# Optimization experiments

Measured on AMD Instinct MI355X. Metric: run time of the kernel, lower is better.

Reference implementation:

```python
import jax, jax.numpy as jnp
import numpy as np

A, B, D, H, O = 64, 4096, 50, 192, 3

def _xavier(key, shape, gain=0.5):
    fan_in, fan_out = shape[-1], shape[-2]
    limit = gain * np.sqrt(6.0 / (fan_in + fan_out))
    return jax.random.uniform(key, shape, jnp.float32, -limit, limit)

def setup_inputs() -> dict:
    key = jax.random.key(0)
    ks = jax.random.split(key, 12)
    return {
        "x": jax.random.normal(ks[0], (B, D), jnp.float32),
        "input_norm_weight": _xavier(ks[1], (A, D)),
        "input_norm_bias": jnp.zeros((A, D), jnp.float32),
        "layer1_weight": _xavier(ks[2], (A, H, D)),
        "layer1_bias": jnp.zeros((A, H), jnp.float32),
        "layer2_weight": _xavier(ks[3], (A, H, H)),
        "layer2_bias": jnp.zeros((A, H), jnp.float32),
        "layer3_weight": _xavier(ks[4], (A, H, H)),
        "layer3_bias": jnp.zeros((A, H), jnp.float32),
        "output_weight": _xavier(ks[5], (A, O, H)),
        "output_bias": jnp.zeros((A, O), jnp.float32),
        "skip1_weight": _xavier(ks[6], (A, H, D)),
        "skip1_bias": jnp.zeros((A, H), jnp.float32),
        "skip2_weight": _xavier(ks[7], (A, H, H)),
        "skip2_bias": jnp.zeros((A, H), jnp.float32),
        "hidden_norm_weight": _xavier(ks[8], (A, H)),
        "hidden_norm_bias": jnp.zeros((A, H), jnp.float32),
    }

def reference(x, input_norm_weight, input_norm_bias,
              layer1_weight, layer1_bias, layer2_weight, layer2_bias,
              layer3_weight, layer3_bias, output_weight, output_bias,
              skip1_weight, skip1_bias, skip2_weight, skip2_bias,
              hidden_norm_weight, hidden_norm_bias):
    # NOTE: the vectorized ensemble's "norms" are affine-only (no mean/var), per source.
    # x: [B, D] -> broadcast over agents: [A, B, D]
    x_norm = x[None, :, :] * input_norm_weight[:, None, :] + input_norm_bias[:, None, :]
    gelu = lambda t: jax.nn.gelu(t, approximate=False)  # torch F.gelu exact
    # per-agent GEMMs: [A,B,in] x [A,out,in] -> [A,B,out]
    h1 = gelu(jnp.einsum('abi,ahi->abh', x_norm, layer1_weight) + layer1_bias[:, None, :]) \
         + jnp.einsum('abi,ahi->abh', x_norm, skip1_weight) + skip1_bias[:, None, :]
    h2 = gelu(jnp.einsum('abi,ahi->abh', h1, layer2_weight) + layer2_bias[:, None, :]) \
         + jnp.einsum('abi,ahi->abh', h1, skip2_weight) + skip2_bias[:, None, :]
    h3 = jnp.einsum('abi,ahi->abh', h2, layer3_weight) + layer3_bias[:, None, :] + h2
    h3 = h3 * hidden_norm_weight[:, None, :] + hidden_norm_bias[:, None, :]
    logits = jnp.einsum('abh,aoh->abo', h3, output_weight) + output_bias[:, None, :]
    return logits  # [A, B, O]
```

## Files before the change

### kernel.cpp

```cpp
#include <hip/hip_runtime.h>
#include <math.h>

#define A_N 64
#define B_N 4096
#define D_N 50
#define H_N 192
#define O_N 3

typedef __attribute__((ext_vector_type(8))) __bf16 bf16x8;
typedef __attribute__((ext_vector_type(4))) __bf16 bf16x4;
typedef __attribute__((ext_vector_type(4))) float f32x4;

#define W1_OFF   0
#define S1_OFF   786432
#define W2_OFF   1572864
#define S2_OFF   3932160
#define W3_OFF   6291456
#define OW_OFF   8650752
#define WS_ELEMS 8847360

#if __has_builtin(__builtin_amdgcn_rcpf)
#define FRCP(x) __builtin_amdgcn_rcpf(x)
#else
#define FRCP(x) (1.0f / (x))
#endif
#if __has_builtin(__builtin_amdgcn_exp2f)
#define FEXP2(x) __builtin_amdgcn_exp2f(x)
#else
#define FEXP2(x) exp2f(x)
#endif

__device__ __forceinline__ float gelu_f(float xx) {
    float t  = 0.70710678118654752440f * xx;
    float at = fabsf(t);
    float k  = FRCP(fmaf(0.3275911f, at, 1.0f));
    float p  = fmaf(k, 1.061405429f, -1.453152027f);
    p = fmaf(k, p, 1.421413741f);
    p = fmaf(k, p, -0.284496736f);
    p = fmaf(k, p, 0.254829592f);
    p = p * k;
    float e  = FEXP2(t * t * -1.44269504088896340736f);
    float er = fmaf(-p, e, 1.0f);
    er = (t < 0.f) ? -er : er;
    return 0.5f * xx * (1.0f + er);
}

__global__ __launch_bounds__(256)
void prep_kernel(const float* __restrict__ w1, const float* __restrict__ s1,
                 const float* __restrict__ w2, const float* __restrict__ s2,
                 const float* __restrict__ w3, const float* __restrict__ ow,
                 __bf16* __restrict__ ws) {
    __shared__ __bf16 T[192 * 72];
    const int b   = blockIdx.x;
    const int tid = threadIdx.x;

    if (b < 1152) {
        int m  = b / 384;
        int r  = b % 384;
        int a  = r / 6;
        int rc = r % 6;
        const float* src = ((m == 0) ? w2 : (m == 1) ? s2 : w3) + (size_t)a * 36864;
        __bf16* dst = ws + ((m == 0) ? W2_OFF : (m == 1) ? S2_OFF : W3_OFF) + (size_t)a * 36864;
        #pragma unroll
        for (int i = 0; i < 6; ++i) {
            int f4 = i * 256 + tid;
            int row = f4 / 48, kc = (f4 % 48) * 4;
            f32x4 v = *(const f32x4*)(src + (size_t)(rc * 32 + row) * 192 + kc);
            bf16x4 o;
            #pragma unroll
            for (int j = 0; j < 4; ++j) o[j] = (__bf16)v[j];
            *(bf16x4*)(T + row * 200 + kc) = o;
        }
        __syncthreads();
        #pragma unroll
        for (int i = 0; i < 3; ++i) {
            int fr = i * 256 + tid;
            int f = fr >> 6, lane = fr & 63;
            int ntl = f / 6, ks = f % 6;
            int n = ntl * 16 + (lane & 15), k = ks * 32 + (lane >> 4) * 8;
            bf16x8 v = *(const bf16x8*)(T + n * 200 + k);
            *(bf16x8*)(dst + ((size_t)(rc * 2 + ntl) * 6 + ks) * 512 + lane * 8) = v;
        }
    } else if (b < 1280) {
        int r = b - 1152; int m = r >> 6; int a = r & 63;
        const float* src = (m ? s1 : w1) + (size_t)a * 9600;
        __bf16* dst = ws + (m ? S1_OFF : W1_OFF) + (size_t)a * 12288;
        for (int e = tid; e < 192 * 72; e += 256) T[e] = (__bf16)0.f;
        __syncthreads();
        for (int e = tid; e < 9600; e += 256) {
            int row = e / 50, k = e - row * 50;
            T[row * 72 + k] = (__bf16)src[e];
        }
        __syncthreads();
        #pragma unroll
        for (int i = 0; i < 6; ++i) {
            int fr = i * 256 + tid;
            int f = fr >> 6, lane = fr & 63;
            int nt = f >> 1, ks = f & 1;
            int n = nt * 16 + (lane & 15), k = ks * 32 + (lane >> 4) * 8;
            bf16x8 v = *(const bf16x8*)(T + n * 72 + k);
            *(bf16x8*)(dst + (size_t)(nt * 2 + ks) * 512 + lane * 8) = v;
        }
    } else {
        int r = b - 1280;
        #pragma unroll
        for (int i = 0; i < 8; ++i) {
            int fr = (r * 8 + i) * 256 + tid;
            int a = fr / 384, rem = fr - a * 384;
            int ks = rem >> 6, lane = rem & 63;
            int n = lane & 15, k = ks * 32 + (lane >> 4) * 8;
            bf16x8 v;
            if (n < O_N) {
                const float* p = ow + ((size_t)a * O_N + n) * H_N + k;
                f32x4 f0 = *(const f32x4*)p, f1 = *(const f32x4*)(p + 4);
                #pragma unroll
                for (int j = 0; j < 4; ++j) { v[j] = (__bf16)f0[j]; v[4 + j] = (__bf16)f1[j]; }
            } else {
                #pragma unroll
                for (int j = 0; j < 8; ++j) v[j] = (__bf16)0.f;
            }
            *(bf16x8*)(ws + OW_OFF + (size_t)a * 3072 + ks * 512 + lane * 8) = v;
        }
    }
}

#define MFMA(a, b, c) __builtin_amdgcn_mfma_f32_16x16x32_bf16((a), (b), (c), 0, 0, 0)

__global__ __launch_bounds__(256, 3)
void srek_mfma(const float* __restrict__ x,
               const float* __restrict__ inw, const float* __restrict__ inb,
               const float* __restrict__ b1,  const float* __restrict__ b2,
               const float* __restrict__ b3,  const float* __restrict__ s1b,
               const float* __restrict__ s2b, const float* __restrict__ hnw,
               const float* __restrict__ hnb, const float* __restrict__ ob,
               const __bf16* __restrict__ ws, float* __restrict__ out) {
    __shared__ __bf16 Xs[8 * 512];
    __shared__ __bf16 Hs[24 * 512];

    const int bid  = blockIdx.x;
    const int slot = bid >> 3;
    const int tile = slot & 63;
    const int a    = ((bid & 7) << 3) | (slot >> 6);
    const int row0 = tile * 64;

    const int tid  = threadIdx.x;
    const int lane = tid & 63;
    const int wv   = tid >> 6;
    const int ln   = lane & 15;
    const int quad = lane >> 4;
    const int aH   = a * H_N;
    const int c0   = wv * 48;
    const int l8   = lane * 8;
    const int f3   = wv * 3;

    const __bf16* W1 = ws + W1_OFF + (size_t)a * 12288;
    const __bf16* S1 = ws + S1_OFF + (size_t)a * 12288;
    const __bf16* W2 = ws + W2_OFF + (size_t)a * 36864;
    const __bf16* S2 = ws + S2_OFF + (size_t)a * 36864;
    const __bf16* W3 = ws + W3_OFF + (size_t)a * 36864;
    const __bf16* OWp= ws + OW_OFF + (size_t)a * 3072;

    bf16x8 nxt[6];
    f32x4 accT[12], accS[12], h2f[12];
    const f32x4 zero = {0.f, 0.f, 0.f, 0.f};

    #pragma unroll
    for (int t = 0; t < 3; ++t) {
        nxt[t]     = *(const bf16x8*)(W1 + ((f3 + t) * 2 + 0) * 512 + l8);
        nxt[3 + t] = *(const bf16x8*)(S1 + ((f3 + t) * 2 + 0) * 512 + l8);
    }

    for (int e = tid; e < 8 * 512; e += 256) {
        int j   = e & 7;
        int lnn = (e >> 3) & 15;
        int qd  = (e >> 7) & 3;
        int kss = (e >> 9) & 1;
        int mtt = (e >> 10) & 3;
        int r = mtt * 16 + lnn;
        int k = kss * 32 + qd * 8 + j;
        float v = 0.f;
        if (k < D_N) v = x[(size_t)(row0 + r) * D_N + k] * inw[a * D_N + k] + inb[a * D_N + k];
        Xs[e] = (__bf16)v;
    }

    auto compute_dual = [&](const __bf16* As, int KS, int ks,
                            const bf16x8* cw, const bf16x8* cs) {
        #pragma unroll
        for (int mt = 0; mt < 4; ++mt) {
            bf16x8 av = *(const bf16x8*)(As + (mt * KS + ks) * 512 + l8);
            #pragma unroll
            for (int t = 0; t < 3; ++t) {
                accT[mt * 3 + t] = MFMA(cw[t], av, accT[mt * 3 + t]);
                accS[mt * 3 + t] = MFMA(cs[t], av, accS[mt * 3 + t]);
            }
        }
    };
    auto compute_single = [&](int ks, const bf16x8* cw) {
        #pragma unroll
        for (int mt = 0; mt < 4; ++mt) {
            bf16x8 av = *(const bf16x8*)(Hs + (mt * 6 + ks) * 512 + l8);
            #pragma unroll
            for (int t = 0; t < 3; ++t)
                accT[mt * 3 + t] = MFMA(cw[t], av, accT[mt * 3 + t]);
        }
    };
    auto store_fragmajor = [&](const f32x4* src) {
        #pragma unroll
        for (int t = 0; t < 3; ++t) {
            int ks2 = (3 * wv + t) >> 1;
            int qp  = (6 * wv + 2 * t + (quad >> 1)) & 3;
            int off = (qp * 16 + ln) * 8 + (quad & 1) * 4;
            #pragma unroll
            for (int mt = 0; mt < 4; ++mt) {
                bf16x4 o;
                #pragma unroll
                for (int rg = 0; rg < 4; ++rg) o[rg] = (__bf16)src[mt * 3 + t][rg];
                *(bf16x4*)(Hs + (mt * 6 + ks2) * 512 + off) = o;
            }
        }
    };

    #pragma unroll
    for (int i = 0; i < 12; ++i) { accT[i] = zero; accS[i] = zero; }
    __syncthreads();

    {
        bf16x8 cw[3], cs[3];
        #pragma unroll
        for (int t = 0; t < 3; ++t) { cw[t] = nxt[t]; cs[t] = nxt[3 + t]; }
        #pragma unroll
        for (int t = 0; t < 3; ++t) {
            nxt[t]     = *(const bf16x8*)(W1 + ((f3 + t) * 2 + 1) * 512 + l8);
            nxt[3 + t] = *(const bf16x8*)(S1 + ((f3 + t) * 2 + 1) * 512 + l8);
        }
        compute_dual(Xs, 2, 0, cw, cs);
        #pragma unroll
        for (int t = 0; t < 3; ++t) { cw[t] = nxt[t]; cs[t] = nxt[3 + t]; }
        #pragma unroll
        for (int t = 0; t < 3; ++t) {
            nxt[t]     = *(const bf16x8*)(W2 + ((f3 + t) * 6 + 0) * 512 + l8);
            nxt[3 + t] = *(const bf16x8*)(S2 + ((f3 + t) * 6 + 0) * 512 + l8);
        }
        compute_dual(Xs, 2, 1, cw, cs);
    }
    #pragma unroll
    for (int t = 0; t < 3; ++t) {
        int colb = c0 + t * 16 + quad * 4;
        f32x4 bb = *(const f32x4*)(b1 + aH + colb);
        f32x4 sb = *(const f32x4*)(s1b + aH + colb);
        #pragma unroll
        for (int mt = 0; mt < 4; ++mt)
            #pragma unroll
            for (int rg = 0; rg < 4; ++rg)
                h2f[mt * 3 + t][rg] = gelu_f(accT[mt * 3 + t][rg] + bb[rg]) + accS[mt * 3 + t][rg] + sb[rg];
    }
    store_fragmajor(h2f);
    #pragma unroll
    for (int i = 0; i < 12; ++i) { accT[i] = zero; accS[i] = zero; }
    __syncthreads();

    #pragma unroll
    for (int ks = 0; ks < 6; ++ks) {
        bf16x8 cw[3], cs[3];
        #pragma unroll
        for (int t = 0; t < 3; ++t) { cw[t] = nxt[t]; cs[t] = nxt[3 + t]; }
        if (ks < 5) {
            #pragma unroll
            for (int t = 0; t < 3; ++t) {
                nxt[t]     = *(const bf16x8*)(W2 + ((f3 + t) * 6 + ks + 1) * 512 + l8);
                nxt[3 + t] = *(const bf16x8*)(S2 + ((f3 + t) * 6 + ks + 1) * 512 + l8);
            }
        } else {
            #pragma unroll
            for (int t = 0; t < 3; ++t)
                nxt[t] = *(const bf16x8*)(W3 + ((f3 + t) * 6 + 0) * 512 + l8);
        }
        compute_dual(Hs, 6, ks, cw, cs);
    }
    #pragma unroll
    for (int t = 0; t < 3; ++t) {
        int colb = c0 + t * 16 + quad * 4;
        f32x4 bb = *(const f32x4*)(b2 + aH + colb);
        f32x4 sb = *(const f32x4*)(s2b + aH + colb);
        #pragma unroll
        for (int mt = 0; mt < 4; ++mt)
            #pragma unroll
            for (int rg = 0; rg < 4; ++rg)
                h2f[mt * 3 + t][rg] = gelu_f(accT[mt * 3 + t][rg] + bb[rg]) + accS[mt * 3 + t][rg] + sb[rg];
    }
    #pragma unroll
    for (int i = 0; i < 12; ++i) accT[i] = zero;
    __syncthreads();
    store_fragmajor(h2f);
    __syncthreads();

    bf16x8 ow6[6];
    #pragma unroll
    for (int ks = 0; ks < 6; ++ks) {
        bf16x8 cw[3];
        #pragma unroll
        for (int t = 0; t < 3; ++t) cw[t] = nxt[t];
        if (ks < 5) {
            #pragma unroll
            for (int t = 0; t < 3; ++t)
                nxt[t] = *(const bf16x8*)(W3 + ((f3 + t) * 6 + ks + 1) * 512 + l8);
        } else {
            #pragma unroll
            for (int kk = 0; kk < 6; ++kk)
                ow6[kk] = *(const bf16x8*)(OWp + kk * 512 + l8);
        }
        compute_single(ks, cw);
    }
    #pragma unroll
    for (int t = 0; t < 3; ++t) {
        int colb = c0 + t * 16 + quad * 4;
        f32x4 b3v = *(const f32x4*)(b3  + aH + colb);
        f32x4 nwv = *(const f32x4*)(hnw + aH + colb);
        f32x4 nbv = *(const f32x4*)(hnb + aH + colb);
        #pragma unroll
        for (int mt = 0; mt < 4; ++mt)
            #pragma unroll
            for (int rg = 0; rg < 4; ++rg)
                h2f[mt * 3 + t][rg] = fmaf(accT[mt * 3 + t][rg] + b3v[rg] + h2f[mt * 3 + t][rg],
                                           nwv[rg], nbv[rg]);
    }
    __syncthreads();
    store_fragmajor(h2f);
    __syncthreads();

    {
        f32x4 acco = zero;
        #pragma unroll
        for (int ks = 0; ks < 6; ++ks) {
            bf16x8 av = *(const bf16x8*)(Hs + (wv * 6 + ks) * 512 + l8);
            acco = MFMA(ow6[ks], av, acco);
        }
        if (quad == 0) {
            float* po = out + ((size_t)a * B_N + row0 + wv * 16 + ln) * O_N;
            po[0] = acco[0] + ob[a * O_N + 0];
            po[1] = acco[1] + ob[a * O_N + 1];
            po[2] = acco[2] + ob[a * O_N + 2];
        }
    }
}

extern "C" void kernel_launch(void* const* d_in, const int* in_sizes, int n_in,
                              void* d_out, int out_size, void* d_ws, size_t ws_size,
                              hipStream_t stream) {
    const float* x   = (const float*)d_in[0];
    const float* inw = (const float*)d_in[1];
    const float* inb = (const float*)d_in[2];
    const float* w1  = (const float*)d_in[3];
    const float* b1  = (const float*)d_in[4];
    const float* w2  = (const float*)d_in[5];
    const float* b2  = (const float*)d_in[6];
    const float* w3  = (const float*)d_in[7];
    const float* b3  = (const float*)d_in[8];
    const float* ow  = (const float*)d_in[9];
    const float* ob  = (const float*)d_in[10];
    const float* s1w = (const float*)d_in[11];
    const float* s1b = (const float*)d_in[12];
    const float* s2w = (const float*)d_in[13];
    const float* s2b = (const float*)d_in[14];
    const float* hnw = (const float*)d_in[15];
    const float* hnb = (const float*)d_in[16];

    __bf16* ws = (__bf16*)d_ws;

    prep_kernel<<<dim3(1292), dim3(256), 0, stream>>>(w1, s1w, w2, s2w, w3, ow, ws);

    srek_mfma<<<dim3(A_N * (B_N / 64)), dim3(256), 0, stream>>>(
        x, inw, inb, b1, b2, b3, s1b, s2b, hnw, hnb, ob, ws, (float*)d_out);
}
```

Before: 225.7 us.

## Load layer2/skip2/layer3 weights as fp32 directly in main kernel, drop prep repack

Removes the prep-kernel conversion of the 192x192 weight matrices to bf16 fragment-major layout. The main kernel now loads fp32 weights straight from the original row-major tensors and converts them to bf16 in registers before each MFMA. This shrinks the prep launch and the workspace, but doubles the bytes each block reads for these weights, adds conversion ALU work, and raises register pressure from the extra fp32 prefetch buffers.

```diff
diff --git a/kernel.cpp b/kernel.cpp
--- a/kernel.cpp
+++ b/kernel.cpp
@@ -13,11 +13,8 @@
 
 #define W1_OFF   0
 #define S1_OFF   786432
-#define W2_OFF   1572864
-#define S2_OFF   3932160
-#define W3_OFF   6291456
-#define OW_OFF   8650752
-#define WS_ELEMS 8847360
+#define OW_OFF   1572864
+#define WS_ELEMS 1769472
 
 #if __has_builtin(__builtin_amdgcn_rcpf)
 #define FRCP(x) __builtin_amdgcn_rcpf(x)
@@ -45,44 +42,22 @@
     return 0.5f * xx * (1.0f + er);
 }
 
+__device__ __forceinline__ bf16x8 cvt8(f32x4 lo, f32x4 hi) {
+    bf16x8 r;
+    #pragma unroll
+    for (int j = 0; j < 4; ++j) { r[j] = (__bf16)lo[j]; r[4 + j] = (__bf16)hi[j]; }
+    return r;
+}
+
 __global__ __launch_bounds__(256)
 void prep_kernel(const float* __restrict__ w1, const float* __restrict__ s1,
-                 const float* __restrict__ w2, const float* __restrict__ s2,
-                 const float* __restrict__ w3, const float* __restrict__ ow,
-                 __bf16* __restrict__ ws) {
+                 const float* __restrict__ ow, __bf16* __restrict__ ws) {
     __shared__ __bf16 T[192 * 72];
     const int b   = blockIdx.x;
     const int tid = threadIdx.x;
 
-    if (b < 1152) {
-        int m  = b / 384;
-        int r  = b % 384;
-        int a  = r / 6;
-        int rc = r % 6;
-        const float* src = ((m == 0) ? w2 : (m == 1) ? s2 : w3) + (size_t)a * 36864;
-        __bf16* dst = ws + ((m == 0) ? W2_OFF : (m == 1) ? S2_OFF : W3_OFF) + (size_t)a * 36864;
-        #pragma unroll
-        for (int i = 0; i < 6; ++i) {
-            int f4 = i * 256 + tid;
-            int row = f4 / 48, kc = (f4 % 48) * 4;
-            f32x4 v = *(const f32x4*)(src + (size_t)(rc * 32 + row) * 192 + kc);
-            bf16x4 o;
-            #pragma unroll
-            for (int j = 0; j < 4; ++j) o[j] = (__bf16)v[j];
-            *(bf16x4*)(T + row * 200 + kc) = o;
-        }
-        __syncthreads();
-        #pragma unroll
-        for (int i = 0; i < 3; ++i) {
-            int fr = i * 256 + tid;
-            int f = fr >> 6, lane = fr & 63;
-            int ntl = f / 6, ks = f % 6;
-            int n = ntl * 16 + (lane & 15), k = ks * 32 + (lane >> 4) * 8;
-            bf16x8 v = *(const bf16x8*)(T + n * 200 + k);
-            *(bf16x8*)(dst + ((size_t)(rc * 2 + ntl) * 6 + ks) * 512 + lane * 8) = v;
-        }
-    } else if (b < 1280) {
-        int r = b - 1152; int m = r >> 6; int a = r & 63;
+    if (b < 128) {
+        int m = b >> 6; int a = b & 63;
         const float* src = (m ? s1 : w1) + (size_t)a * 9600;
         __bf16* dst = ws + (m ? S1_OFF : W1_OFF) + (size_t)a * 12288;
         for (int e = tid; e < 192 * 72; e += 256) T[e] = (__bf16)0.f;
@@ -102,7 +77,7 @@
             *(bf16x8*)(dst + (size_t)(nt * 2 + ks) * 512 + lane * 8) = v;
         }
     } else {
-        int r = b - 1280;
+        int r = b - 128;
         #pragma unroll
         for (int i = 0; i < 8; ++i) {
             int fr = (r * 8 + i) * 256 + tid;
@@ -133,6 +108,8 @@
                const float* __restrict__ b3,  const float* __restrict__ s1b,
                const float* __restrict__ s2b, const float* __restrict__ hnw,
                const float* __restrict__ hnb, const float* __restrict__ ob,
+               const float* __restrict__ w2,  const float* __restrict__ s2,
+               const float* __restrict__ w3,
                const __bf16* __restrict__ ws, float* __restrict__ out) {
     __shared__ __bf16 Xs[8 * 512];
     __shared__ __bf16 Hs[24 * 512];
@@ -155,12 +132,13 @@
 
     const __bf16* W1 = ws + W1_OFF + (size_t)a * 12288;
     const __bf16* S1 = ws + S1_OFF + (size_t)a * 12288;
-    const __bf16* W2 = ws + W2_OFF + (size_t)a * 36864;
-    const __bf16* S2 = ws + S2_OFF + (size_t)a * 36864;
-    const __bf16* W3 = ws + W3_OFF + (size_t)a * 36864;
     const __bf16* OWp= ws + OW_OFF + (size_t)a * 3072;
+    const float* W2f = w2 + (size_t)a * 36864 + (size_t)(f3 * 16 + ln) * 192 + quad * 8;
+    const float* S2f = s2 + (size_t)a * 36864 + (size_t)(f3 * 16 + ln) * 192 + quad * 8;
+    const float* W3f = w3 + (size_t)a * 36864 + (size_t)(f3 * 16 + ln) * 192 + quad * 8;
 
     bf16x8 nxt[6];
+    f32x4 nf[6];
     f32x4 accT[12], accS[12], h2f[12];
     const f32x4 zero = {0.f, 0.f, 0.f, 0.f};
 
@@ -238,8 +216,9 @@
         for (int t = 0; t < 3; ++t) { cw[t] = nxt[t]; cs[t] = nxt[3 + t]; }
         #pragma unroll
         for (int t = 0; t < 3; ++t) {
-            nxt[t]     = *(const bf16x8*)(W2 + ((f3 + t) * 6 + 0) * 512 + l8);
-            nxt[3 + t] = *(const bf16x8*)(S2 + ((f3 + t) * 6 + 0) * 512 + l8);
+            const float* p = W2f + t * 3072;
+            nf[2 * t]     = *(const f32x4*)p;
+            nf[2 * t + 1] = *(const f32x4*)(p + 4);
         }
         compute_dual(Xs, 2, 1, cw, cs);
     }
@@ -261,21 +240,48 @@
 
     #pragma unroll
     for (int ks = 0; ks < 6; ++ks) {
-        bf16x8 cw[3], cs[3];
-        #pragma unroll
-        for (int t = 0; t < 3; ++t) { cw[t] = nxt[t]; cs[t] = nxt[3 + t]; }
+        f32x4 sf[6];
+        #pragma unroll
+        for (int t = 0; t < 3; ++t) {
+            const float* p = S2f + t * 3072 + ks * 32;
+            sf[2 * t]     = *(const f32x4*)p;
+            sf[2 * t + 1] = *(const f32x4*)(p + 4);
+        }
+        bf16x8 cw[3];
+        #pragma unroll
+        for (int t = 0; t < 3; ++t) cw[t] = cvt8(nf[2 * t], nf[2 * t + 1]);
         if (ks < 5) {
             #pragma unroll
             for (int t = 0; t < 3; ++t) {
-                nxt[t]     = *(const bf16x8*)(W2 + ((f3 + t) * 6 + ks + 1) * 512 + l8);
-                nxt[3 + t] = *(const bf16x8*)(S2 + ((f3 + t) * 6 + ks + 1) * 512 + l8);
+                const float* p = W2f + t * 3072 + (ks + 1) * 32;
+                nf[2 * t]     = *(const f32x4*)p;
+                nf[2 * t + 1] = *(const f32x4*)(p + 4);
             }
         } else {
             #pragma unroll
+            for (int t = 0; t < 3; ++t) {
+                const float* p = W3f + t * 3072;
+                nf[2 * t]     = *(const f32x4*)p;
+                nf[2 * t + 1] = *(const f32x4*)(p + 4);
+            }
+        }
+        #pragma unroll
+        for (int mt = 0; mt < 4; ++mt) {
+            bf16x8 av = *(const bf16x8*)(Hs + (mt * 6 + ks) * 512 + l8);
+            #pragma unroll
             for (int t = 0; t < 3; ++t)
-                nxt[t] = *(const bf16x8*)(W3 + ((f3 + t) * 6 + 0) * 512 + l8);
-        }
-        compute_dual(Hs, 6, ks, cw, cs);
+                accT[mt * 3 + t] = MFMA(cw[t], av, accT[mt * 3 + t]);
+        }
+        bf16x8 cs[3];
+        #pragma unroll
+        for (int t = 0; t < 3; ++t) cs[t] = cvt8(sf[2 * t], sf[2 * t + 1]);
+        #pragma unroll
+        for (int mt = 0; mt < 4; ++mt) {
+            bf16x8 av = *(const bf16x8*)(Hs + (mt * 6 + ks) * 512 + l8);
+            #pragma unroll
+            for (int t = 0; t < 3; ++t)
+                accS[mt * 3 + t] = MFMA(cs[t], av, accS[mt * 3 + t]);
+        }
     }
     #pragma unroll
     for (int t = 0; t < 3; ++t) {
@@ -299,11 +305,14 @@
     for (int ks = 0; ks < 6; ++ks) {
         bf16x8 cw[3];
         #pragma unroll
-        for (int t = 0; t < 3; ++t) cw[t] = nxt[t];
+        for (int t = 0; t < 3; ++t) cw[t] = cvt8(nf[2 * t], nf[2 * t + 1]);
         if (ks < 5) {
             #pragma unroll
-            for (int t = 0; t < 3; ++t)
-                nxt[t] = *(const bf16x8*)(W3 + ((f3 + t) * 6 + ks + 1) * 512 + l8);
+            for (int t = 0; t < 3; ++t) {
+                const float* p = W3f + t * 3072 + (ks + 1) * 32;
+                nf[2 * t]     = *(const f32x4*)p;
+                nf[2 * t + 1] = *(const f32x4*)(p + 4);
+            }
         } else {
             #pragma unroll
             for (int kk = 0; kk < 6; ++kk)
@@ -367,8 +376,8 @@
 
     __bf16* ws = (__bf16*)d_ws;
 
-    prep_kernel<<<dim3(1292), dim3(256), 0, stream>>>(w1, s1w, w2, s2w, w3, ow, ws);
+    prep_kernel<<<dim3(140), dim3(256), 0, stream>>>(w1, s1w, ow, ws);
 
     srek_mfma<<<dim3(A_N * (B_N / 64)), dim3(256), 0, stream>>>(
-        x, inw, inb, b1, b2, b3, s1b, s2b, hnw, hnb, ob, ws, (float*)d_out);
-}
+        x, inw, inb, b1, b2, b3, s1b, s2b, hnw, hnb, ob, w2, s2w, w3, ws, (float*)d_out);
+}
```

New measurement: 352.0 us. 1.56x slower.
